# Performance work log

Measured on AMD Instinct MI355X. Metric: run time of the kernel, lower is better.

Reference implementation:

```python
import jax, jax.numpy as jnp
import numpy as np
import math

NCLASSES = 3
NMS_THR = 0.25
SCORE_THR = 0.1
MAX_NUM = 500
B, N = 4, 8192


def setup_inputs() -> dict:
    key = jax.random.key(0)
    ks = jax.random.split(key, 6)
    xy = jax.random.uniform(ks[0], (B, N, 2), minval=0.0, maxval=70.0)
    z = jax.random.normal(ks[1], (B, N, 1))
    lwh = jax.random.uniform(ks[2], (B, N, 3), minval=1.0, maxval=5.0)
    theta = jax.random.uniform(ks[3], (B, N, 1), minval=-math.pi, maxval=math.pi)
    cls = jax.random.uniform(ks[4], (B, N, NCLASSES))
    dirc = jax.random.randint(ks[5], (B, N, 1), 0, 2).astype(jnp.float32)
    results = jnp.concatenate([xy, z, lwh, theta, cls, dirc], axis=-1)  # [B,N,11]
    return {"results": results}


def limit_period(val, offset=1.0, period=math.pi):
    return val - jnp.floor(val / period + offset) * period


def _pairwise_iou(b):
    # b: [N,4] = (x1,y1,x2,y2); axis-aligned BEV IoU
    x1, y1, x2, y2 = b[:, 0], b[:, 1], b[:, 2], b[:, 3]
    area = (x2 - x1) * (y2 - y1)  # [N]
    iw = jnp.clip(jnp.minimum(x2[:, None], x2[None, :]) - jnp.maximum(x1[:, None], x1[None, :]), 0.0)
    ih = jnp.clip(jnp.minimum(y2[:, None], y2[None, :]) - jnp.maximum(y1[:, None], y1[None, :]), 0.0)
    inter = iw * ih
    return inter / (area[:, None] + area[None, :] - inter + 1e-8)


def _nms_class(boxes4, scores):
    # greedy NMS on score-descending order; invalid (below-threshold) boxes get -inf score
    valid = scores > SCORE_THR
    s = jnp.where(valid, scores, -jnp.inf)
    order = jnp.argsort(-s)  # descending
    bs = boxes4[order]
    ss = s[order]
    iou = _pairwise_iou(bs)  # [N,N]
    idx = jnp.arange(boxes4.shape[0])
    keep0 = jnp.isfinite(ss)

    def body(i, keep):
        sup = keep[i] & (iou[i] > NMS_THR) & (idx > i)
        return keep & ~sup

    keep = jax.lax.fori_loop(0, boxes4.shape[0], body, keep0)
    return order, jnp.where(keep, ss, -jnp.inf)


def _process(sample):
    # sample: [N,11] -> padded (bboxes [MAX_NUM,7], labels [MAX_NUM], scores [MAX_NUM])
    bbox = sample[:, :7]
    cls = sample[:, 7:10]
    dirp = sample[:, 10]
    xy = bbox[:, :2]
    lw = bbox[:, 3:5]
    boxes4 = jnp.concatenate([xy - lw / 2, xy + lw / 2], axis=-1)  # [N,4]

    all_b, all_l, all_s = [], [], []
    for c in range(NCLASSES):
        order, ss = _nms_class(boxes4, cls[:, c])
        bb = bbox[order]
        dd = dirp[order]
        ang = limit_period(bb[:, 6]) + (1.0 - dd) * math.pi
        bb = jnp.concatenate([bb[:, :6], ang[:, None]], axis=-1)
        all_b.append(bb)
        all_s.append(ss)
        all_l.append(jnp.full((N,), c, dtype=jnp.int32))
    b = jnp.concatenate(all_b, 0)   # [3N,7]
    s = jnp.concatenate(all_s, 0)   # [3N]
    l = jnp.concatenate(all_l, 0)   # [3N]
    top_s, top_i = jax.lax.top_k(s, MAX_NUM)
    return b[top_i], l[top_i], top_s


def reference(results):
    # results: [B,N,11]; returns (lidar_bboxes [B,500,7], labels [B,500], scores [B,500])
    return jax.vmap(_process)(results)
```

## Files before the change

kernel.cpp:

```cpp
#include <hip/hip_runtime.h>
#include <stdint.h>

#pragma clang fp contract(off)

#define NB 4
#define NN 8192
#define NC 3
#define NG 12
#define MAXN 500
#define KEEP_CAP 512

typedef unsigned long long u64;
typedef uint32_t u32;
typedef uint16_t u16;

#define NSO   0u
#define NSKEY 393216u
#define NSB4  786432u
#define NSAR  2359296u
#define NVAL  2752512u
#define NALV  2764800u
#define NKKEY 2777088u
#define NKPOS 2801664u
#define NKCNT 2826240u
#define NFLG  2826304u
#define PMAT  3145728u
#define NMAT  9437184u
#define MATB  8388608ull

#define PR_CH   32
#define PR_ROWS 2048
#define PUNITS_PER_G 528
#define PB_TPB 256
#define PB_BLOCKS 1584

#define WS_SORTED_ORIG 0
#define WS_ALIVE       393216
#define WS_KEPT_KEY    405504
#define WS_KEPT_POS    430080
#define WS_KEPT_CNT    454656
#define NMS_EPS 1.0000004f

__device__ __forceinline__ u32 sort_key(float s) {
  u32 b = __float_as_uint(s);
  u32 o = (b & 0x80000000u) ? ~b : (b | 0x80000000u);
  return ~o;
}

#define PHYS(i) ((i) + ((i) >> 3))
#define CEX(A, B, UP) \
  { if ((x[A] > x[B]) == (UP)) { u64 tt = x[A]; x[A] = x[B]; x[B] = tt; } }

__global__ __launch_bounds__(256) void sortL_kernel(
    const float* __restrict__ in, u64* __restrict__ kk)
{
  const int g = blockIdx.x >> 2, seg = blockIdx.x & 3;
  const int b = g / NC, c = g % NC;
  const float* __restrict__ base = in + (size_t)b * NN * 11;
  __shared__ u64 sk[2304];
  const int tid = threadIdx.x;
  const int gbase = seg << 11;

  for (int i = tid; i < 2048; i += 256) {
    int p = gbase + i;
    float sc = base[p * 11 + 7 + c];
    float s = (sc > 0.1f) ? sc : -INFINITY;
    sk[PHYS(i)] = ((u64)sort_key(s) << 16) | (u32)p;
  }
  __syncthreads();
  {
    const int pb = 9 * tid;
    u64 x[8];
#pragma unroll
    for (int a = 0; a < 8; ++a) x[a] = sk[pb + a];
    const bool u8 = (((gbase + (tid << 3)) & 8) == 0);
    CEX(0, 1, true); CEX(2, 3, false); CEX(4, 5, true); CEX(6, 7, false);
    CEX(0, 2, true); CEX(1, 3, true); CEX(4, 6, false); CEX(5, 7, false);
    CEX(0, 1, true); CEX(2, 3, true); CEX(4, 5, false); CEX(6, 7, false);
    CEX(0, 4, u8); CEX(1, 5, u8); CEX(2, 6, u8); CEX(3, 7, u8);
    CEX(0, 2, u8); CEX(1, 3, u8); CEX(4, 6, u8); CEX(5, 7, u8);
    CEX(0, 1, u8); CEX(2, 3, u8); CEX(4, 5, u8); CEX(6, 7, u8);
#pragma unroll
    for (int a = 0; a < 8; ++a) sk[pb + a] = x[a];
  }
  __syncthreads();
  for (int k = 16; k <= 2048; k <<= 1) {
    for (int j = k >> 1; j >= 8; j >>= 1) {
      for (int t = tid; t < 1024; t += 256) {
        int i = (t << 1) - (t & (j - 1));
        int q = i | j;
        int pi = PHYS(i), pq = PHYS(q);
        u64 ka = sk[pi], kb = sk[pq];
        bool up = (((gbase + i) & k) == 0);
        if ((ka > kb) == up) { sk[pi] = kb; sk[pq] = ka; }
      }
      __syncthreads();
    }
    {
      const int lb = tid << 3;
      const bool up = (((gbase + lb) & k) == 0);
      const int pb = 9 * tid;
      u64 x[8];
#pragma unroll
      for (int a = 0; a < 8; ++a) x[a] = sk[pb + a];
      CEX(0, 4, up); CEX(1, 5, up); CEX(2, 6, up); CEX(3, 7, up);
      CEX(0, 2, up); CEX(1, 3, up); CEX(4, 6, up); CEX(5, 7, up);
      CEX(0, 1, up); CEX(2, 3, up); CEX(4, 5, up); CEX(6, 7, up);
#pragma unroll
      for (int a = 0; a < 8; ++a) sk[pb + a] = x[a];
    }
    __syncthreads();
  }
  for (int i = tid; i < 2048; i += 256)
    kk[(size_t)g * NN + gbase + i] = sk[PHYS(i)];
}

__global__ __launch_bounds__(512) void sortX1_kernel(u64* __restrict__ kk)
{
  const int g = blockIdx.x >> 1, pr = blockIdx.x & 1;
  const size_t off = (size_t)g * NN + pr * 4096;
  __shared__ u64 sk[4608];
  const int tid = threadIdx.x;
  const bool up = (pr == 0);

  for (int i = tid; i < 4096; i += 512) sk[PHYS(i)] = kk[off + i];
  __syncthreads();
  for (int j = 2048; j >= 8; j >>= 1) {
    for (int t = tid; t < 2048; t += 512) {
      int i = (t << 1) - (t & (j - 1));
      int q = i | j;
      int pi = PHYS(i), pq = PHYS(q);
      u64 ka = sk[pi], kb = sk[pq];
      if ((ka > kb) == up) { sk[pi] = kb; sk[pq] = ka; }
    }
    __syncthreads();
  }
  {
    const int pb = 9 * tid;
    u64 x[8];
#pragma unroll
    for (int a = 0; a < 8; ++a) x[a] = sk[pb + a];
    CEX(0, 4, up); CEX(1, 5, up); CEX(2, 6, up); CEX(3, 7, up);
    CEX(0, 2, up); CEX(1, 3, up); CEX(4, 6, up); CEX(5, 7, up);
    CEX(0, 1, up); CEX(2, 3, up); CEX(4, 5, up); CEX(6, 7, up);
#pragma unroll
    for (int a = 0; a < 8; ++a) sk[pb + a] = x[a];
  }
  __syncthreads();
  for (int i = tid; i < 4096; i += 512) kk[off + i] = sk[PHYS(i)];
}

__global__ __launch_bounds__(1024) void sortX2_kernel(u64* __restrict__ kk)
{
  const int g = blockIdx.x >> 2;
  const int i = ((blockIdx.x & 3) << 10) + threadIdx.x;
  u64* p = kk + (size_t)g * NN;
  u64 a = p[i], b = p[i + 4096];
  if (a > b) { p[i] = b; p[i + 4096] = a; }
}

__global__ __launch_bounds__(512) void sortX3_kernel(
    const float* __restrict__ in, u64* __restrict__ kk, u32* __restrict__ so,
    u32* __restrict__ skey, float4* __restrict__ sb4, float* __restrict__ sar,
    u64* __restrict__ valid)
{
  const int g = blockIdx.x >> 1, half = blockIdx.x & 1;
  const int b = g / NC;
  const size_t off = (size_t)g * NN + half * 4096;
  const int pbase = half * 4096;
  __shared__ u64 sk[4608];
  const int tid = threadIdx.x;

  for (int i = tid; i < 4096; i += 512) sk[PHYS(i)] = kk[off + i];
  __syncthreads();
  for (int j = 2048; j >= 8; j >>= 1) {
    for (int t = tid; t < 2048; t += 512) {
      int i = (t << 1) - (t & (j - 1));
      int q = i | j;
      int pi = PHYS(i), pq = PHYS(q);
      u64 ka = sk[pi], kb = sk[pq];
      if (ka > kb) { sk[pi] = kb; sk[pq] = ka; }
    }
    __syncthreads();
  }
  {
    const int pb = 9 * tid;
    u64 x[8];
#pragma unroll
    for (int a = 0; a < 8; ++a) x[a] = sk[pb + a];
    CEX(0, 4, true); CEX(1, 5, true); CEX(2, 6, true); CEX(3, 7, true);
    CEX(0, 2, true); CEX(1, 3, true); CEX(4, 6, true); CEX(5, 7, true);
    CEX(0, 1, true); CEX(2, 3, true); CEX(4, 5, true); CEX(6, 7, true);
#pragma unroll
    for (int a = 0; a < 8; ++a) sk[pb + a] = x[a];
  }
  __syncthreads();

  const float* __restrict__ base = in + (size_t)b * NN * 11;
  const int lane = tid & 63;
#pragma unroll
  for (int it = 0; it < 8; ++it) {
    int i = it * 512 + tid;
    int p = pbase + i;
    u64 kv = sk[PHYS(i)];
    int orig = (int)(kv & 0xFFFFu);
    u32 key32 = (u32)(kv >> 16);
    so[(size_t)g * NN + p] = (u32)orig;
    skey[(size_t)g * NN + p] = key32;
    const float* r = base + orig * 11;
    float x = r[0], y = r[1], l = r[3], wd = r[4];
    float hx = l * 0.5f, hy = wd * 0.5f;
    float x1 = x - hx, y1 = y - hy, x2 = x + hx, y2 = y + hy;
    sb4[(size_t)g * NN + p] = make_float4(x1, y1, x2, y2);
    sar[(size_t)g * NN + p] = (x2 - x1) * (y2 - y1);
    u64 bal = __ballot(key32 != 0xFF800000u);
    if (lane == 0) valid[g * 128 + (p >> 6)] = bal;
  }
}

__global__ __launch_bounds__(PB_TPB) void build_prefix_kernel(
    const float4* __restrict__ sb4, const float* __restrict__ sar,
    u64* __restrict__ pmat)
{
  const int wib = __builtin_amdgcn_readfirstlane((int)(threadIdx.x >> 6));
  const int lane = threadIdx.x & 63;
  const int W = blockIdx.x * (PB_TPB / 64) + wib;
  if (W >= NG * PUNITS_PER_G) return;
  const int g = W / PUNITS_PER_G;
  int r = W - g * PUNITS_PER_G;
  int rb = 0, cum = 0;
  while (r >= cum + (PR_CH - rb)) { cum += PR_CH - rb; ++rb; }
  const int jw = rb + (r - cum);
  const double CMULT = 0.25 * (1.0 + 0x1p-24);

  const int col = jw * 64 + lane;
  const float4 J = sb4[(size_t)g * NN + col];
  const float jar = sar[(size_t)g * NN + col];
  const float4* __restrict__ Ib = sb4 + (size_t)g * NN + rb * 64;
  const float* __restrict__ Ia = sar + (size_t)g * NN + rb * 64;

  u32 accLo = 0, accHi = 0;
  for (int rr = 0; rr < 64; ++rr) {
    const float4 I = Ib[rr];
    const float iar = Ia[rr];
    const bool sel = (lane == rr);
    float iw = fminf(I.z, J.z) - fmaxf(I.x, J.x);
    float ih = fminf(I.w, J.w) - fmaxf(I.y, J.y);
    iw = fmaxf(iw, 0.0f); ih = fmaxf(ih, 0.0f);
    float inter = iw * ih;
    float denom = ((iar + jar) - inter) + 1e-8f;
    u64 cand = __ballot((double)inter > CMULT * (double)denom);
    accLo = sel ? (u32)(cand & 0xffffffffu) : accLo;
    accHi = sel ? (u32)(cand >> 32) : accHi;
  }
  pmat[((size_t)(g * PR_CH + jw)) * PR_ROWS + rb * 64 + lane] =
      ((u64)accHi << 32) | accLo;
}

__global__ __launch_bounds__(1024) void scan_prefix_kernel(
    const u64* __restrict__ pmat, const u64* __restrict__ valid,
    const u32* __restrict__ skey, u32* __restrict__ kept_key,
    u32* __restrict__ kept_pos, u32* __restrict__ kept_cnt,
    u32* __restrict__ flags)
{
  const int g = blockIdx.x;
  const int tid = threadIdx.x;
  const int wv = tid >> 6, lane = tid & 63;
  const int wl = tid & 127, grp = tid >> 7;
  __shared__ u64 remv[PR_CH];
  __shared__ u64 keepw[PR_CH];
  __shared__ u64 keepS;
  __shared__ u32 prefixL[PR_CH];
  __shared__ u32 cntS;
  __shared__ int stopS;

  if (tid < PR_CH) { remv[tid] = ~valid[g * 128 + tid]; keepw[tid] = 0; }
  if (tid == 0) { cntS = 0; stopS = 0; }
  __syncthreads();

  const u64* __restrict__ pm = pmat + (size_t)g * PR_CH * PR_ROWS;
  u64 rwDiag = 0, rwDiagNext = 0;
  if (wv == 0) rwDiag = pm[lane];
  const u64 maskgt = (lane == 63) ? 0ull : (~0ull << (lane + 1));

  for (int cc = 0; cc < PR_CH; ++cc) {
    const int w = cc + 1 + wl;
    const bool act = (w < PR_CH);
    u64 rw[8];
    if (act) {
#pragma unroll
      for (int k = 0; k < 8; ++k)
        rw[k] = pm[(size_t)w * PR_ROWS + cc * 64 + grp * 8 + k];
    }
    if (wv == 0) {
      const u64 alive0 = ~remv[cc];
      u64 K = alive0;
      for (int it = 0; it < 64; ++it) {
        u64 contrib = ((K >> lane) & 1ull) ? (rwDiag & maskgt) : 0ull;
#pragma unroll
        for (int off = 32; off > 0; off >>= 1)
          contrib |= (u64)__shfl_xor((long long)contrib, off);
        u64 Knew = alive0 & ~contrib;
        if (Knew == K) break;
        K = Knew;
      }
      if (lane == 0) {
        keepw[cc] = K; keepS = K;
        cntS += (u32)__popcll(K);
        if (cntS >= KEEP_CAP) stopS = 1;
      }
      if (cc + 1 < PR_CH)
        rwDiagNext = pm[(size_t)(cc + 1) * PR_ROWS + (cc + 1) * 64 + lane];
    }
    __syncthreads();
    if (stopS) break;
    if (act) {
      const u32 kmg = (u32)((keepS >> (grp * 8)) & 0xffu);
      u64 acc = 0;
#pragma unroll
      for (int k = 0; k < 8; ++k)
        if ((kmg >> k) & 1u) acc |= rw[k];
      if (acc) atomicOr(&remv[w], acc);
    }
    if (wv == 0) rwDiag = rwDiagNext;
    __syncthreads();
  }
  __syncthreads();

  if (tid == 0) {
    u32 acc = 0;
    for (int i = 0; i < PR_CH; ++i) { prefixL[i] = acc; acc += (u32)__popcll(keepw[i]); }
    cntS = acc;
    u32 ok = (acc >= KEEP_CAP) ? 1u : 0u;
    flags[g] = ok;
    if (ok) kept_cnt[g] = KEEP_CAP;
  }
  __syncthreads();
  if (cntS < KEEP_CAP) return;
  for (int p = tid; p < PR_ROWS; p += 1024) {
    int wd = p >> 6;
    u64 kw = keepw[wd];
    if ((kw >> (p & 63)) & 1ull) {
      u32 rank = prefixL[wd] + (u32)__popcll(kw & ((1ull << (p & 63)) - 1ull));
      if (rank < KEEP_CAP) {
        kept_key[g * KEEP_CAP + rank] = skey[g * NN + p];
        kept_pos[g * KEEP_CAP + rank] = (u32)p;
      }
    }
  }
}

#define UNITS_PER_G 1088
#define BUILD_TPB 256
#define BUILD_BLOCKS 816

__global__ __launch_bounds__(BUILD_TPB) void build_kernel(
    const float4* __restrict__ sb4, const float* __restrict__ sar,
    u64* __restrict__ mat, const u32* __restrict__ flags, int g0, int P)
{
  const int wib = __builtin_amdgcn_readfirstlane((int)(threadIdx.x >> 6));
  const int lane = threadIdx.x & 63;
  const int W = blockIdx.x * (BUILD_TPB / 64) + wib;
  const int NUNITS = P * UNITS_PER_G;
  const double CMULT = 0.25 * (1.0 + 0x1p-24);

  for (int u = W; u < NUNITS; u += BUILD_BLOCKS * (BUILD_TPB / 64)) {
    const int gp = u / UNITS_PER_G;
    if (flags[g0 + gp]) continue;
    int r = u - gp * UNITS_PER_G;
    int rb8 = 0, cum = 0;
    while (r >= cum + 8 * (16 - rb8)) { cum += 8 * (16 - rb8); ++rb8; }
    const int idx = r - cum;
    const int nb = 16 - rb8;
    const int rb = rb8 * 8 + idx / nb;
    const int jb = rb8 + idx % nb;

    const int g = g0 + gp;
    float jx1[8], jy1[8], jx2[8], jy2[8], jar[8];
#pragma unroll
    for (int wq = 0; wq < 8; ++wq) {
      const int col = jb * 512 + wq * 64 + lane;
      const float4 J = sb4[(size_t)g * NN + col];
      jx1[wq] = J.x; jy1[wq] = J.y; jx2[wq] = J.z; jy2[wq] = J.w;
      jar[wq] = sar[(size_t)g * NN + col];
    }
    u32 accLo[8], accHi[8];
#pragma unroll
    for (int wq = 0; wq < 8; ++wq) { accLo[wq] = 0u; accHi[wq] = 0u; }

    const float4* __restrict__ Ib = sb4 + (size_t)g * NN + rb * 64;
    const float* __restrict__ Ia = sar + (size_t)g * NN + rb * 64;

    for (int rr = 0; rr < 64; ++rr) {
      const float4 I = Ib[rr];
      const float iar = Ia[rr];
      const bool sel = (lane == rr);
#pragma unroll
      for (int wq = 0; wq < 8; ++wq) {
        float iw = fminf(I.z, jx2[wq]) - fmaxf(I.x, jx1[wq]);
        float ih = fminf(I.w, jy2[wq]) - fmaxf(I.y, jy1[wq]);
        iw = fmaxf(iw, 0.0f); ih = fmaxf(ih, 0.0f);
        float inter = iw * ih;
        float denom = ((iar + jar[wq]) - inter) + 1e-8f;
        u64 cand = __ballot((double)inter > CMULT * (double)denom);
        accLo[wq] = sel ? (u32)(cand & 0xffffffffu) : accLo[wq];
        accHi[wq] = sel ? (u32)(cand >> 32) : accHi[wq];
      }
    }
    u64* dst = mat + ((size_t)(gp * NN + rb * 64 + lane)) * 128 + jb * 8;
    uint4* d4 = (uint4*)dst;
    d4[0] = make_uint4(accLo[0], accHi[0], accLo[1], accHi[1]);
    d4[1] = make_uint4(accLo[2], accHi[2], accLo[3], accHi[3]);
    d4[2] = make_uint4(accLo[4], accHi[4], accLo[5], accHi[5]);
    d4[3] = make_uint4(accLo[6], accHi[6], accLo[7], accHi[7]);
  }
}

__global__ __launch_bounds__(1024) void scan_kernel(
    const u64* __restrict__ mat, const u64* __restrict__ valid,
    const u32* __restrict__ skey, u64* __restrict__ alive_out,
    u32* __restrict__ kept_key, u32* __restrict__ kept_pos,
    u32* __restrict__ kept_cnt, const u32* __restrict__ flags, int g0)
{
  const int gp = blockIdx.x, g = g0 + gp;
  if (flags[g]) return;
  const int tid = threadIdx.x;
  const int wv = tid >> 6, lane = tid & 63;
  const int wl = tid & 127, grp = tid >> 7;
  __shared__ u64 remv[128];
  __shared__ u64 keepw[128];
  __shared__ u64 keepS;
  __shared__ u32 prefixL[128];

  if (tid < 128) remv[tid] = ~valid[g * 128 + tid];
  __syncthreads();

  const u64* __restrict__ pm = mat + (size_t)gp * NN * 128;
  u64 rwDiag = 0, rwDiagNext = 0;
  if (wv == 0) rwDiag = pm[((size_t)lane) * 128 + 0];

  for (int cc = 0; cc < 128; ++cc) {
    const int w = cc + 1 + wl;
    const bool act = (w < 128);
    u64 rw[8];
    if (act) {
#pragma unroll
      for (int k = 0; k < 8; ++k)
        rw[k] = pm[((size_t)(cc * 64 + grp * 8 + k)) * 128 + w];
    }
    if (wv == 0) {
      u64 m = ~remv[cc];
      u64 keepm = 0;
      while (m) {
        int bp = __ffsll(m) - 1;
        keepm |= 1ull << bp;
        m &= ~(1ull << bp);
        u32 rlo = (u32)__builtin_amdgcn_readlane((int)(u32)(rwDiag & 0xffffffffu), bp);
        u32 rhi = (u32)__builtin_amdgcn_readlane((int)(u32)(rwDiag >> 32), bp);
        m &= ~(((u64)rhi << 32) | rlo);
      }
      if (lane == 0) { keepw[cc] = keepm; keepS = keepm; }
      if (cc + 1 < 128) rwDiagNext = pm[((size_t)((cc + 1) * 64 + lane)) * 128 + (cc + 1)];
    }
    __syncthreads();
    if (act) {
      const u32 kmg = (u32)((keepS >> (grp * 8)) & 0xffu);
      u64 acc = 0;
#pragma unroll
      for (int k = 0; k < 8; ++k)
        if ((kmg >> k) & 1u) acc |= rw[k];
      if (acc) atomicOr(&remv[w], acc);
    }
    if (wv == 0) rwDiag = rwDiagNext;
    __syncthreads();
  }

  if (tid == 0) {
    u32 acc = 0;
    for (int i = 0; i < 128; ++i) { prefixL[i] = acc; acc += (u32)__popcll(keepw[i]); }
    kept_cnt[g] = acc;
  }
  __syncthreads();
  if (tid < 128) alive_out[g * 128 + tid] = keepw[tid];
  for (int p = tid; p < NN; p += 1024) {
    int wd = p >> 6;
    u64 kw = keepw[wd];
    if ((kw >> (p & 63)) & 1ull) {
      u32 rank = prefixL[wd] + (u32)__popcll(kw & ((1ull << (p & 63)) - 1ull));
      if (rank < KEEP_CAP) {
        kept_key[g * KEEP_CAP + rank] = skey[g * NN + p];
        kept_pos[g * KEEP_CAP + rank] = (u32)p;
      }
    }
  }
}

__global__ __launch_bounds__(1024) void nms_kernel(
    const float* __restrict__ in, u32* __restrict__ sorted_orig,
    u64* __restrict__ alive_out, u32* __restrict__ kept_key,
    u32* __restrict__ kept_pos, u32* __restrict__ kept_cnt)
{
  const int g = blockIdx.x;
  const int b = g / NC, c = g % NC;
  const float* __restrict__ base = in + (size_t)b * NN * 11;
  __shared__ u32 keys[NN];
  __shared__ uint16_t sidx[NN];
  __shared__ float4 keeperBuf[2][64];
  __shared__ int nkBuf[2];
  __shared__ u64 aliveArr[128];
  __shared__ u32 prefix[128];
  const int tid = threadIdx.x;
  const int w = tid >> 6, lane = tid & 63;

  for (int p = tid; p < NN; p += 1024) {
    float sc = base[p * 11 + 7 + c];
    float s = (sc > 0.1f) ? sc : -INFINITY;
    keys[p] = sort_key(s);
    sidx[p] = (uint16_t)p;
  }
  __syncthreads();
  for (int k = 2; k <= NN; k <<= 1) {
    for (int j = k >> 1; j > 0; j >>= 1) {
      for (int t = tid; t < NN / 2; t += 1024) {
        int i = (t << 1) - (t & (j - 1));
        int q = i | j;
        u32 ka = keys[i], kb = keys[q];
        uint16_t ia = sidx[i], ib = sidx[q];
        bool gt = (ka > kb) || (ka == kb && ia > ib);
        bool up = ((i & k) == 0);
        if (gt == up) { keys[i] = kb; keys[q] = ka; sidx[i] = ib; sidx[q] = ia; }
      }
      __syncthreads();
    }
  }
  float bx1[8], by1[8], bx2[8], by2[8], barea[8];
  u64 alive[8];
#pragma unroll
  for (int k = 0; k < 8; ++k) {
    int p = k * 1024 + tid;
    u32 key = keys[p];
    int orig = sidx[p];
    sorted_orig[g * NN + p] = (u32)orig;
    const float* r = base + orig * 11;
    float x = r[0], y = r[1], l = r[3], wd = r[4];
    float hx = l * 0.5f, hy = wd * 0.5f;
    bx1[k] = x - hx; by1[k] = y - hy; bx2[k] = x + hx; by2[k] = y + hy;
    barea[k] = (bx2[k] - bx1[k]) * (by2[k] - by1[k]);
    alive[k] = __ballot(key != 0xFF800000u);
  }
  for (int cc = 0; cc < 128; ++cc) {
    __syncthreads();
    int nk_prev = (cc > 0) ? nkBuf[(cc - 1) & 1] : 0;
    if (nk_prev > 0) {
      const int par = (cc - 1) & 1;
      for (int j = 0; j < nk_prev; ++j) {
        float4 K = keeperBuf[par][j];
        float ka = (K.z - K.x) * (K.w - K.y);
#pragma unroll
        for (int k = 0; k < 8; ++k) {
          if ((k * 16 + w) < cc) continue;
          if (alive[k] == 0ull) continue;
          float iw = fminf(bx2[k], K.z) - fmaxf(bx1[k], K.x);
          float ih = fminf(by2[k], K.w) - fmaxf(by1[k], K.y);
          iw = fmaxf(iw, 0.0f); ih = fmaxf(ih, 0.0f);
          float inter = iw * ih;
          float denom = (barea[k] + ka) - inter + 1e-8f;
          float t = 0.25f * denom;
          u64 sup = __ballot(inter > t);
          u64 wnd = __ballot(inter > t && inter <= t * NMS_EPS);
          if (wnd) {
            bool bb = inter > t;
            if (bb && inter <= t * NMS_EPS) bb = (inter / denom) > 0.25f;
            sup = __ballot(bb);
          }
          alive[k] &= ~sup;
        }
      }
    }
    if (w == (cc & 15)) {
      float mx1 = 0.f, my1 = 0.f, mx2 = 0.f, my2 = 0.f, ma = 0.f;
      u64 m = 0ull;
#pragma unroll
      for (int k = 0; k < 8; ++k) if (k == (cc >> 4)) {
        mx1 = bx1[k]; my1 = by1[k]; mx2 = bx2[k]; my2 = by2[k]; ma = barea[k];
        m = alive[k];
      }
      u64 keepm = 0ull;
      int nk = 0;
      while (m) {
        int bp = __ffsll(m) - 1;
        keepm |= 1ull << bp;
        m &= ~(1ull << bp);
        float kx1 = __shfl(mx1, bp), ky1 = __shfl(my1, bp);
        float kx2 = __shfl(mx2, bp), ky2 = __shfl(my2, bp);
        float ka = (kx2 - kx1) * (ky2 - ky1);
        float iw = fminf(mx2, kx2) - fmaxf(mx1, kx1);
        float ih = fminf(my2, ky2) - fmaxf(my1, ky1);
        iw = fmaxf(iw, 0.0f); ih = fmaxf(ih, 0.0f);
        float inter = iw * ih;
        float denom = (ma + ka) - inter + 1e-8f;
        float t = 0.25f * denom;
        u64 sup = __ballot(inter > t);
        u64 wnd = __ballot(inter > t && inter <= t * NMS_EPS);
        if (wnd) {
          bool bb = inter > t;
          if (bb && inter <= t * NMS_EPS) bb = (inter / denom) > 0.25f;
          sup = __ballot(bb);
        }
        m &= ~sup;
        if (lane == bp) keeperBuf[cc & 1][nk] = make_float4(mx1, my1, mx2, my2);
        nk++;
      }
#pragma unroll
      for (int k = 0; k < 8; ++k) if (k == (cc >> 4)) alive[k] = keepm;
      if (lane == 0) nkBuf[cc & 1] = nk;
    }
  }
  __syncthreads();
  if (lane == 0) {
#pragma unroll
    for (int k = 0; k < 8; ++k) aliveArr[k * 16 + w] = alive[k];
  }
  __syncthreads();
  if (tid == 0) {
    u32 acc = 0;
    for (int i = 0; i < 128; ++i) { prefix[i] = acc; acc += (u32)__popcll(aliveArr[i]); }
    kept_cnt[g] = acc;
  }
  __syncthreads();
  for (int i = tid; i < 128; i += 1024) alive_out[g * 128 + i] = aliveArr[i];
#pragma unroll
  for (int k = 0; k < 8; ++k) {
    int word = k * 16 + w;
    u64 a = alive[k];
    if ((a >> lane) & 1ull) {
      u32 rank = prefix[word] + (u32)__popcll(a & ((1ull << lane) - 1ull));
      if (rank < KEEP_CAP) {
        int p = k * 1024 + tid;
        kept_key[g * KEEP_CAP + rank] = keys[p];
        kept_pos[g * KEEP_CAP + rank] = (u32)p;
      }
    }
  }
}

__global__ __launch_bounds__(512) void topk_kernel(
    const float* __restrict__ in, const u32* __restrict__ sorted_orig,
    const u64* __restrict__ alive_ws, const u32* __restrict__ kept_key,
    const u32* __restrict__ kept_pos, const u32* __restrict__ kept_cnt,
    float* __restrict__ out)
{
  const int b = blockIdx.x;
  const int tid = threadIdx.x;
  __shared__ u64 arr[NC][KEEP_CAP];
  __shared__ int sT[3], sL[3];
  if (tid < 3) {
    int K = (int)kept_cnt[b * 3 + tid];
    sT[tid] = K;
    sL[tid] = min(K, KEEP_CAP);
  }
  __syncthreads();
  const int L0 = sL[0], L1 = sL[1], L2 = sL[2];
  const int navail = L0 + L1 + L2;
  const int Ttot = sT[0] + sT[1] + sT[2];

  for (int s = tid; s < NC * KEEP_CAP; s += 512) {
    int c = s >> 9, i = s & 511;
    u64 key = ~0ull;
    if (i < sL[c]) {
      int g = b * 3 + c;
      u64 k32 = kept_key[g * KEEP_CAP + i];
      u32 pos = kept_pos[g * KEEP_CAP + i];
      key = (k32 << 15) | (u32)(c * NN + pos);
    }
    arr[c][i] = key;
  }
  __syncthreads();

  for (int s = tid; s < NC * KEEP_CAP; s += 512) {
    int c = s >> 9, i = s & 511;
    if (i >= sL[c]) continue;
    u64 k = arr[c][i];
    int rank = i;
#pragma unroll
    for (int oc = 0; oc < NC; ++oc) {
      if (oc == c) continue;
      int lo = 0, hi = sL[oc];
      while (lo < hi) { int mid = (lo + hi) >> 1; if (arr[oc][mid] < k) lo = mid + 1; else hi = mid; }
      rank += lo;
    }
    if (rank < MAXN) {
      u32 flat = (u32)(k & 32767u);
      int cc = (int)(flat >> 13), pos = (int)(flat & 8191);
      u32 k32 = (u32)(k >> 15);
      u32 o = ~k32;
      u32 bits = (o & 0x80000000u) ? (o ^ 0x80000000u) : ~o;
      float sval = __uint_as_float(bits);
      u32 orig = sorted_orig[(b * 3 + cc) * NN + pos];
      const float* row = in + ((size_t)b * NN + orig) * 11;
      const float PI_F = 3.14159265358979323846f;
      float theta = row[6];
      float v = theta / PI_F;
      float fl = floorf(v + 1.0f);
      float lp = theta - fl * PI_F;
      float ang = lp + (1.0f - row[10]) * PI_F;
      float* ob = out + ((size_t)b * MAXN + rank) * 7;
      ob[0] = row[0]; ob[1] = row[1]; ob[2] = row[2];
      ob[3] = row[3]; ob[4] = row[4]; ob[5] = row[5]; ob[6] = ang;
      out[NB * MAXN * 7 + b * MAXN + rank] = (float)cc;
      out[NB * MAXN * 7 + NB * MAXN + b * MAXN + rank] = sval;
    }
  }

  for (int r = navail + tid; r < MAXN; r += 512) {
    int need = r - Ttot;
    int fflat = 0;
    for (int wd = 0; wd < 384; ++wd) {
      u64 a = alive_ws[b * 384 + wd];
      int z = 64 - __popcll(a);
      if (need < z) {
        u64 na = ~a;
        for (int it = 0; it < need; ++it) na &= na - 1ull;
        fflat = wd * 64 + (__ffsll(na) - 1);
        break;
      }
      need -= z;
    }
    int c = fflat >> 13, pos = fflat & 8191;
    u32 orig = sorted_orig[(b * 3 + c) * NN + pos];
    const float* row = in + ((size_t)b * NN + orig) * 11;
    const float PI_F = 3.14159265358979323846f;
    float theta = row[6];
    float v = theta / PI_F;
    float fl = floorf(v + 1.0f);
    float lp = theta - fl * PI_F;
    float ang = lp + (1.0f - row[10]) * PI_F;
    float* ob = out + ((size_t)b * MAXN + r) * 7;
    ob[0] = row[0]; ob[1] = row[1]; ob[2] = row[2];
    ob[3] = row[3]; ob[4] = row[4]; ob[5] = row[5]; ob[6] = ang;
    out[NB * MAXN * 7 + b * MAXN + r] = (float)c;
    out[NB * MAXN * 7 + NB * MAXN + b * MAXN + r] = -INFINITY;
  }
}

extern "C" void kernel_launch(void* const* d_in, const int* in_sizes, int n_in,
                              void* d_out, int out_size, void* d_ws, size_t ws_size,
                              hipStream_t stream) {
  const float* in = (const float*)d_in[0];
  float* out = (float*)d_out;
  char* ws = (char*)d_ws;

  int P = 0;
  const int cands[6] = {12, 6, 4, 3, 2, 1};
  for (int ci = 0; ci < 6; ++ci) {
    if ((size_t)NMAT + (size_t)cands[ci] * MATB <= ws_size) { P = cands[ci]; break; }
  }

  if (P > 0) {
    u32* so = (u32*)(ws + NSO);
    u32* skey = (u32*)(ws + NSKEY);
    float4* sb4 = (float4*)(ws + NSB4);
    float* sar = (float*)(ws + NSAR);
    u64* valid = (u64*)(ws + NVAL);
    u64* alive = (u64*)(ws + NALV);
    u32* kkey = (u32*)(ws + NKKEY);
    u32* kpos = (u32*)(ws + NKPOS);
    u32* kcnt = (u32*)(ws + NKCNT);
    u32* flags = (u32*)(ws + NFLG);
    u64* pmat = (u64*)(ws + PMAT);
    u64* kk = (u64*)(ws + PMAT);
    u64* mat = (u64*)(ws + NMAT);

    sortL_kernel<<<dim3(48), dim3(256), 0, stream>>>(in, kk);
    sortX1_kernel<<<dim3(24), dim3(512), 0, stream>>>(kk);
    sortX2_kernel<<<dim3(48), dim3(1024), 0, stream>>>(kk);
    sortX3_kernel<<<dim3(24), dim3(512), 0, stream>>>(
        in, kk, so, skey, sb4, sar, valid);
    build_prefix_kernel<<<dim3(PB_BLOCKS), dim3(PB_TPB), 0, stream>>>(
        sb4, sar, pmat);
    scan_prefix_kernel<<<dim3(NG), dim3(1024), 0, stream>>>(
        pmat, valid, skey, kkey, kpos, kcnt, flags);
    for (int g0 = 0; g0 < NG; g0 += P) {
      build_kernel<<<dim3(BUILD_BLOCKS), dim3(BUILD_TPB), 0, stream>>>(
          sb4, sar, mat, flags, g0, P);
      scan_kernel<<<dim3(P), dim3(1024), 0, stream>>>(
          mat, valid, skey, alive, kkey, kpos, kcnt, flags, g0);
    }
    topk_kernel<<<dim3(NB), dim3(512), 0, stream>>>(
        in, so, alive, kkey, kpos, kcnt, out);
  } else {
    u32* sorted_orig = (u32*)(ws + WS_SORTED_ORIG);
    u64* alive = (u64*)(ws + WS_ALIVE);
    u32* kept_key = (u32*)(ws + WS_KEPT_KEY);
    u32* kept_pos = (u32*)(ws + WS_KEPT_POS);
    u32* kept_cnt = (u32*)(ws + WS_KEPT_CNT);
    nms_kernel<<<dim3(NG), dim3(1024), 0, stream>>>(
        in, sorted_orig, alive, kept_key, kept_pos, kept_cnt);
    topk_kernel<<<dim3(NB), dim3(512), 0, stream>>>(
        in, sorted_orig, alive, kept_key, kept_pos, kept_cnt, out);
  }
}
```

Before: 110.2 us.

## Replace full sort merge with rank-based top-2048 merge; drop full-matrix NMS fallback

```diff
diff --git a/kernel.cpp b/kernel.cpp
--- a/kernel.cpp
+++ b/kernel.cpp
@@ -12,7 +12,6 @@
 
 typedef unsigned long long u64;
 typedef uint32_t u32;
-typedef uint16_t u16;
 
 #define NSO   0u
 #define NSKEY 393216u
@@ -25,8 +24,7 @@
 #define NKCNT 2826240u
 #define NFLG  2826304u
 #define PMAT  3145728u
-#define NMAT  9437184u
-#define MATB  8388608ull
+#define WS_NEED 9437184u
 
 #define PR_CH   32
 #define PR_ROWS 2048
@@ -73,7 +71,7 @@
     u64 x[8];
 #pragma unroll
     for (int a = 0; a < 8; ++a) x[a] = sk[pb + a];
-    const bool u8 = (((gbase + (tid << 3)) & 8) == 0);
+    const bool u8 = ((((tid << 3)) & 8) == 0);
     CEX(0, 1, true); CEX(2, 3, false); CEX(4, 5, true); CEX(6, 7, false);
     CEX(0, 2, true); CEX(1, 3, true); CEX(4, 6, false); CEX(5, 7, false);
     CEX(0, 1, true); CEX(2, 3, true); CEX(4, 5, false); CEX(6, 7, false);
@@ -91,14 +89,14 @@
         int q = i | j;
         int pi = PHYS(i), pq = PHYS(q);
         u64 ka = sk[pi], kb = sk[pq];
-        bool up = (((gbase + i) & k) == 0);
+        bool up = ((i & k) == 0);
         if ((ka > kb) == up) { sk[pi] = kb; sk[pq] = ka; }
       }
       __syncthreads();
     }
     {
       const int lb = tid << 3;
-      const bool up = (((gbase + lb) & k) == 0);
+      const bool up = ((lb & k) == 0);
       const int pb = 9 * tid;
       u64 x[8];
 #pragma unroll
@@ -115,106 +113,55 @@
     kk[(size_t)g * NN + gbase + i] = sk[PHYS(i)];
 }
 
-__global__ __launch_bounds__(512) void sortX1_kernel(u64* __restrict__ kk)
+__global__ __launch_bounds__(512) void merge_kernel(
+    const float* __restrict__ in, const u64* __restrict__ kk,
+    u32* __restrict__ so, u32* __restrict__ skey, float4* __restrict__ sb4,
+    float* __restrict__ sar, u64* __restrict__ valid)
 {
-  const int g = blockIdx.x >> 1, pr = blockIdx.x & 1;
-  const size_t off = (size_t)g * NN + pr * 4096;
-  __shared__ u64 sk[4608];
+  const int g = blockIdx.x;
+  const int b = g / NC;
   const int tid = threadIdx.x;
-  const bool up = (pr == 0);
-
-  for (int i = tid; i < 4096; i += 512) sk[PHYS(i)] = kk[off + i];
-  __syncthreads();
-  for (int j = 2048; j >= 8; j >>= 1) {
-    for (int t = tid; t < 2048; t += 512) {
-      int i = (t << 1) - (t & (j - 1));
-      int q = i | j;
-      int pi = PHYS(i), pq = PHYS(q);
-      u64 ka = sk[pi], kb = sk[pq];
-      if ((ka > kb) == up) { sk[pi] = kb; sk[pq] = ka; }
-    }
-    __syncthreads();
-  }
-  {
-    const int pb = 9 * tid;
-    u64 x[8];
-#pragma unroll
-    for (int a = 0; a < 8; ++a) x[a] = sk[pb + a];
-    CEX(0, 4, up); CEX(1, 5, up); CEX(2, 6, up); CEX(3, 7, up);
-    CEX(0, 2, up); CEX(1, 3, up); CEX(4, 6, up); CEX(5, 7, up);
-    CEX(0, 1, up); CEX(2, 3, up); CEX(4, 5, up); CEX(6, 7, up);
-#pragma unroll
-    for (int a = 0; a < 8; ++a) sk[pb + a] = x[a];
-  }
-  __syncthreads();
-  for (int i = tid; i < 4096; i += 512) kk[off + i] = sk[PHYS(i)];
-}
-
-__global__ __launch_bounds__(1024) void sortX2_kernel(u64* __restrict__ kk)
-{
-  const int g = blockIdx.x >> 2;
-  const int i = ((blockIdx.x & 3) << 10) + threadIdx.x;
-  u64* p = kk + (size_t)g * NN;
-  u64 a = p[i], b = p[i + 4096];
-  if (a > b) { p[i] = b; p[i + 4096] = a; }
-}
-
-__global__ __launch_bounds__(512) void sortX3_kernel(
-    const float* __restrict__ in, u64* __restrict__ kk, u32* __restrict__ so,
-    u32* __restrict__ skey, float4* __restrict__ sb4, float* __restrict__ sar,
-    u64* __restrict__ valid)
-{
-  const int g = blockIdx.x >> 1, half = blockIdx.x & 1;
-  const int b = g / NC;
-  const size_t off = (size_t)g * NN + half * 4096;
-  const int pbase = half * 4096;
-  __shared__ u64 sk[4608];
-  const int tid = threadIdx.x;
-
-  for (int i = tid; i < 4096; i += 512) sk[PHYS(i)] = kk[off + i];
-  __syncthreads();
-  for (int j = 2048; j >= 8; j >>= 1) {
-    for (int t = tid; t < 2048; t += 512) {
-      int i = (t << 1) - (t & (j - 1));
-      int q = i | j;
-      int pi = PHYS(i), pq = PHYS(q);
-      u64 ka = sk[pi], kb = sk[pq];
-      if (ka > kb) { sk[pi] = kb; sk[pq] = ka; }
-    }
-    __syncthreads();
-  }
-  {
-    const int pb = 9 * tid;
-    u64 x[8];
-#pragma unroll
-    for (int a = 0; a < 8; ++a) x[a] = sk[pb + a];
-    CEX(0, 4, true); CEX(1, 5, true); CEX(2, 6, true); CEX(3, 7, true);
-    CEX(0, 2, true); CEX(1, 3, true); CEX(4, 6, true); CEX(5, 7, true);
-    CEX(0, 1, true); CEX(2, 3, true); CEX(4, 5, true); CEX(6, 7, true);
-#pragma unroll
-    for (int a = 0; a < 8; ++a) sk[pb + a] = x[a];
+  __shared__ u64 outk[PR_ROWS];
+  const u64* __restrict__ ks = kk + (size_t)g * NN;
+
+  for (int e = tid; e < NN; e += 512) {
+    const int seg = e >> 11, idx = e & 2047;
+    const u64 k = ks[e];
+    int rank = idx;
+#pragma unroll
+    for (int os = 0; os < 4; ++os) {
+      if (os == seg) continue;
+      const u64* __restrict__ arr = ks + (os << 11);
+      int pos = 0;
+#pragma unroll
+      for (int st = 1024; st > 0; st >>= 1) {
+        int np = pos + st;
+        if (np <= 2048 && arr[np - 1] < k) pos = np;
+      }
+      rank += pos;
+    }
+    if (rank < PR_ROWS) outk[rank] = k;
   }
   __syncthreads();
 
   const float* __restrict__ base = in + (size_t)b * NN * 11;
   const int lane = tid & 63;
 #pragma unroll
-  for (int it = 0; it < 8; ++it) {
+  for (int it = 0; it < PR_ROWS / 512; ++it) {
     int i = it * 512 + tid;
-    int p = pbase + i;
-    u64 kv = sk[PHYS(i)];
+    u64 kv = outk[i];
     int orig = (int)(kv & 0xFFFFu);
     u32 key32 = (u32)(kv >> 16);
-    so[(size_t)g * NN + p] = (u32)orig;
-    skey[(size_t)g * NN + p] = key32;
+    so[(size_t)g * NN + i] = (u32)orig;
+    skey[(size_t)g * NN + i] = key32;
     const float* r = base + orig * 11;
     float x = r[0], y = r[1], l = r[3], wd = r[4];
     float hx = l * 0.5f, hy = wd * 0.5f;
     float x1 = x - hx, y1 = y - hy, x2 = x + hx, y2 = y + hy;
-    sb4[(size_t)g * NN + p] = make_float4(x1, y1, x2, y2);
-    sar[(size_t)g * NN + p] = (x2 - x1) * (y2 - y1);
+    sb4[(size_t)g * NN + i] = make_float4(x1, y1, x2, y2);
+    sar[(size_t)g * NN + i] = (x2 - x1) * (y2 - y1);
     u64 bal = __ballot(key32 != 0xFF800000u);
-    if (lane == 0) valid[g * 128 + (p >> 6)] = bal;
+    if (lane == 0) valid[g * 128 + (i >> 6)] = bal;
   }
 }
 
@@ -350,157 +297,14 @@
   }
 }
 
-#define UNITS_PER_G 1088
-#define BUILD_TPB 256
-#define BUILD_BLOCKS 816
-
-__global__ __launch_bounds__(BUILD_TPB) void build_kernel(
-    const float4* __restrict__ sb4, const float* __restrict__ sar,
-    u64* __restrict__ mat, const u32* __restrict__ flags, int g0, int P)
-{
-  const int wib = __builtin_amdgcn_readfirstlane((int)(threadIdx.x >> 6));
-  const int lane = threadIdx.x & 63;
-  const int W = blockIdx.x * (BUILD_TPB / 64) + wib;
-  const int NUNITS = P * UNITS_PER_G;
-  const double CMULT = 0.25 * (1.0 + 0x1p-24);
-
-  for (int u = W; u < NUNITS; u += BUILD_BLOCKS * (BUILD_TPB / 64)) {
-    const int gp = u / UNITS_PER_G;
-    if (flags[g0 + gp]) continue;
-    int r = u - gp * UNITS_PER_G;
-    int rb8 = 0, cum = 0;
-    while (r >= cum + 8 * (16 - rb8)) { cum += 8 * (16 - rb8); ++rb8; }
-    const int idx = r - cum;
-    const int nb = 16 - rb8;
-    const int rb = rb8 * 8 + idx / nb;
-    const int jb = rb8 + idx % nb;
-
-    const int g = g0 + gp;
-    float jx1[8], jy1[8], jx2[8], jy2[8], jar[8];
-#pragma unroll
-    for (int wq = 0; wq < 8; ++wq) {
-      const int col = jb * 512 + wq * 64 + lane;
-      const float4 J = sb4[(size_t)g * NN + col];
-      jx1[wq] = J.x; jy1[wq] = J.y; jx2[wq] = J.z; jy2[wq] = J.w;
-      jar[wq] = sar[(size_t)g * NN + col];
-    }
-    u32 accLo[8], accHi[8];
-#pragma unroll
-    for (int wq = 0; wq < 8; ++wq) { accLo[wq] = 0u; accHi[wq] = 0u; }
-
-    const float4* __restrict__ Ib = sb4 + (size_t)g * NN + rb * 64;
-    const float* __restrict__ Ia = sar + (size_t)g * NN + rb * 64;
-
-    for (int rr = 0; rr < 64; ++rr) {
-      const float4 I = Ib[rr];
-      const float iar = Ia[rr];
-      const bool sel = (lane == rr);
-#pragma unroll
-      for (int wq = 0; wq < 8; ++wq) {
-        float iw = fminf(I.z, jx2[wq]) - fmaxf(I.x, jx1[wq]);
-        float ih = fminf(I.w, jy2[wq]) - fmaxf(I.y, jy1[wq]);
-        iw = fmaxf(iw, 0.0f); ih = fmaxf(ih, 0.0f);
-        float inter = iw * ih;
-        float denom = ((iar + jar[wq]) - inter) + 1e-8f;
-        u64 cand = __ballot((double)inter > CMULT * (double)denom);
-        accLo[wq] = sel ? (u32)(cand & 0xffffffffu) : accLo[wq];
-        accHi[wq] = sel ? (u32)(cand >> 32) : accHi[wq];
-      }
-    }
-    u64* dst = mat + ((size_t)(gp * NN + rb * 64 + lane)) * 128 + jb * 8;
-    uint4* d4 = (uint4*)dst;
-    d4[0] = make_uint4(accLo[0], accHi[0], accLo[1], accHi[1]);
-    d4[1] = make_uint4(accLo[2], accHi[2], accLo[3], accHi[3]);
-    d4[2] = make_uint4(accLo[4], accHi[4], accLo[5], accHi[5]);
-    d4[3] = make_uint4(accLo[6], accHi[6], accLo[7], accHi[7]);
-  }
-}
-
-__global__ __launch_bounds__(1024) void scan_kernel(
-    const u64* __restrict__ mat, const u64* __restrict__ valid,
-    const u32* __restrict__ skey, u64* __restrict__ alive_out,
-    u32* __restrict__ kept_key, u32* __restrict__ kept_pos,
-    u32* __restrict__ kept_cnt, const u32* __restrict__ flags, int g0)
-{
-  const int gp = blockIdx.x, g = g0 + gp;
-  if (flags[g]) return;
-  const int tid = threadIdx.x;
-  const int wv = tid >> 6, lane = tid & 63;
-  const int wl = tid & 127, grp = tid >> 7;
-  __shared__ u64 remv[128];
-  __shared__ u64 keepw[128];
-  __shared__ u64 keepS;
-  __shared__ u32 prefixL[128];
-
-  if (tid < 128) remv[tid] = ~valid[g * 128 + tid];
-  __syncthreads();
-
-  const u64* __restrict__ pm = mat + (size_t)gp * NN * 128;
-  u64 rwDiag = 0, rwDiagNext = 0;
-  if (wv == 0) rwDiag = pm[((size_t)lane) * 128 + 0];
-
-  for (int cc = 0; cc < 128; ++cc) {
-    const int w = cc + 1 + wl;
-    const bool act = (w < 128);
-    u64 rw[8];
-    if (act) {
-#pragma unroll
-      for (int k = 0; k < 8; ++k)
-        rw[k] = pm[((size_t)(cc * 64 + grp * 8 + k)) * 128 + w];
-    }
-    if (wv == 0) {
-      u64 m = ~remv[cc];
-      u64 keepm = 0;
-      while (m) {
-        int bp = __ffsll(m) - 1;
-        keepm |= 1ull << bp;
-        m &= ~(1ull << bp);
-        u32 rlo = (u32)__builtin_amdgcn_readlane((int)(u32)(rwDiag & 0xffffffffu), bp);
-        u32 rhi = (u32)__builtin_amdgcn_readlane((int)(u32)(rwDiag >> 32), bp);
-        m &= ~(((u64)rhi << 32) | rlo);
-      }
-      if (lane == 0) { keepw[cc] = keepm; keepS = keepm; }
-      if (cc + 1 < 128) rwDiagNext = pm[((size_t)((cc + 1) * 64 + lane)) * 128 + (cc + 1)];
-    }
-    __syncthreads();
-    if (act) {
-      const u32 kmg = (u32)((keepS >> (grp * 8)) & 0xffu);
-      u64 acc = 0;
-#pragma unroll
-      for (int k = 0; k < 8; ++k)
-        if ((kmg >> k) & 1u) acc |= rw[k];
-      if (acc) atomicOr(&remv[w], acc);
-    }
-    if (wv == 0) rwDiag = rwDiagNext;
-    __syncthreads();
-  }
-
-  if (tid == 0) {
-    u32 acc = 0;
-    for (int i = 0; i < 128; ++i) { prefixL[i] = acc; acc += (u32)__popcll(keepw[i]); }
-    kept_cnt[g] = acc;
-  }
-  __syncthreads();
-  if (tid < 128) alive_out[g * 128 + tid] = keepw[tid];
-  for (int p = tid; p < NN; p += 1024) {
-    int wd = p >> 6;
-    u64 kw = keepw[wd];
-    if ((kw >> (p & 63)) & 1ull) {
-      u32 rank = prefixL[wd] + (u32)__popcll(kw & ((1ull << (p & 63)) - 1ull));
-      if (rank < KEEP_CAP) {
-        kept_key[g * KEEP_CAP + rank] = skey[g * NN + p];
-        kept_pos[g * KEEP_CAP + rank] = (u32)p;
-      }
-    }
-  }
-}
-
 __global__ __launch_bounds__(1024) void nms_kernel(
     const float* __restrict__ in, u32* __restrict__ sorted_orig,
     u64* __restrict__ alive_out, u32* __restrict__ kept_key,
-    u32* __restrict__ kept_pos, u32* __restrict__ kept_cnt)
+    u32* __restrict__ kept_pos, u32* __restrict__ kept_cnt,
+    const u32* __restrict__ flags)
 {
   const int g = blockIdx.x;
+  if (flags != nullptr && flags[g]) return;
   const int b = g / NC, c = g % NC;
   const float* __restrict__ base = in + (size_t)b * NN * 11;
   __shared__ u32 keys[NN];
@@ -750,13 +554,7 @@
   float* out = (float*)d_out;
   char* ws = (char*)d_ws;
 
-  int P = 0;
-  const int cands[6] = {12, 6, 4, 3, 2, 1};
-  for (int ci = 0; ci < 6; ++ci) {
-    if ((size_t)NMAT + (size_t)cands[ci] * MATB <= ws_size) { P = cands[ci]; break; }
-  }
-
-  if (P > 0) {
+  if (ws_size >= (size_t)WS_NEED) {
     u32* so = (u32*)(ws + NSO);
     u32* skey = (u32*)(ws + NSKEY);
     float4* sb4 = (float4*)(ws + NSB4);
@@ -769,23 +567,16 @@
     u32* flags = (u32*)(ws + NFLG);
     u64* pmat = (u64*)(ws + PMAT);
     u64* kk = (u64*)(ws + PMAT);
-    u64* mat = (u64*)(ws + NMAT);
 
     sortL_kernel<<<dim3(48), dim3(256), 0, stream>>>(in, kk);
-    sortX1_kernel<<<dim3(24), dim3(512), 0, stream>>>(kk);
-    sortX2_kernel<<<dim3(48), dim3(1024), 0, stream>>>(kk);
-    sortX3_kernel<<<dim3(24), dim3(512), 0, stream>>>(
+    merge_kernel<<<dim3(NG), dim3(512), 0, stream>>>(
         in, kk, so, skey, sb4, sar, valid);
     build_prefix_kernel<<<dim3(PB_BLOCKS), dim3(PB_TPB), 0, stream>>>(
         sb4, sar, pmat);
     scan_prefix_kernel<<<dim3(NG), dim3(1024), 0, stream>>>(
         pmat, valid, skey, kkey, kpos, kcnt, flags);
-    for (int g0 = 0; g0 < NG; g0 += P) {
-      build_kernel<<<dim3(BUILD_BLOCKS), dim3(BUILD_TPB), 0, stream>>>(
-          sb4, sar, mat, flags, g0, P);
-      scan_kernel<<<dim3(P), dim3(1024), 0, stream>>>(
-          mat, valid, skey, alive, kkey, kpos, kcnt, flags, g0);
-    }
+    nms_kernel<<<dim3(NG), dim3(1024), 0, stream>>>(
+        in, so, alive, kkey, kpos, kcnt, flags);
     topk_kernel<<<dim3(NB), dim3(512), 0, stream>>>(
         in, so, alive, kkey, kpos, kcnt, out);
   } else {
@@ -795,7 +586,7 @@
     u32* kept_pos = (u32*)(ws + WS_KEPT_POS);
     u32* kept_cnt = (u32*)(ws + WS_KEPT_CNT);
     nms_kernel<<<dim3(NG), dim3(1024), 0, stream>>>(
-        in, sorted_orig, alive, kept_key, kept_pos, kept_cnt);
+        in, sorted_orig, alive, kept_key, kept_pos, kept_cnt, nullptr);
     topk_kernel<<<dim3(NB), dim3(512), 0, stream>>>(
         in, sorted_orig, alive, kept_key, kept_pos, kept_cnt, out);
   }
```

Result: slower. 144.8 us (+31.3%).
